# Performance work log

Hardware: AMD Instinct MI355X
Metric: run time of the kernel (lower is better)

The kernel has to match this reference:

```python
import jax, jax.numpy as jnp
from jax import lax
import numpy as np

EPS = 1e-5
N_OBS_STEPS = 2

def _layernorm(x, g, b):
    m = jnp.mean(x, -1, keepdims=True)
    v = jnp.mean((x - m) ** 2, -1, keepdims=True)
    return (x - m) * lax.rsqrt(v + EPS) * g + b

def _fps(pc, num_points):
    # pc: [B, N, 3]; iterative farthest point sampling, start at index 0
    B, N, _ = pc.shape
    dist0 = jnp.full((B, N), jnp.inf, pc.dtype)
    far0 = jnp.zeros((B,), jnp.int32)
    def step(carry, _):
        dist, far = carry
        centroid = jnp.take_along_axis(pc, far[:, None, None], axis=1)  # [B,1,3]
        d = jnp.sum((pc - centroid) ** 2, -1)                            # [B,N]
        dist = jnp.minimum(dist, d)
        nxt = jnp.argmax(dist, -1).astype(jnp.int32)
        return (dist, nxt), far
    _, idx = lax.scan(step, (dist0, far0), None, length=num_points)
    idx = idx.T  # [B, num_points]
    return jnp.take_along_axis(pc, idx[..., None], axis=1)

def setup_inputs() -> dict:
    key = jax.random.key(0)
    ks = jax.random.split(key, 16)
    B, N, S = 256, 8192, 32
    def lin(k, i, o):
        return jax.random.normal(k, (i, o), jnp.float32) / np.sqrt(i)
    inp = {
        'point_cloud': jax.random.normal(ks[0], (B, N, 3), jnp.float32),
        'joint_state': jax.random.normal(ks[1], (B, S), jnp.float32),
        'num_points': 2048,
        'w1': lin(ks[2], 3, 64),   'b1': jnp.zeros((64,)),  'g1': jnp.ones((64,)),  'be1': jnp.zeros((64,)),
        'w2': lin(ks[3], 64, 128), 'b2': jnp.zeros((128,)), 'g2': jnp.ones((128,)), 'be2': jnp.zeros((128,)),
        'w3': lin(ks[4], 128, 256),'b3': jnp.zeros((256,)), 'g3': jnp.ones((256,)), 'be3': jnp.zeros((256,)),
        'wp': lin(ks[5], 256, 64), 'bp': jnp.zeros((64,)),  'gp': jnp.ones((64,)),  'bep': jnp.zeros((64,)),
        'ws1': lin(ks[6], S, 64),  'bs1': jnp.zeros((64,)),
        'ws2': lin(ks[7], 64, 64), 'bs2': jnp.zeros((64,)),
    }
    return inp

def reference(point_cloud, joint_state, num_points,
              w1, b1, g1, be1, w2, b2, g2, be2, w3, b3, g3, be3,
              wp, bp, gp, bep, ws1, bs1, ws2, bs2):
    pc = point_cloud[..., :3]
    pc = _fps(pc, num_points)                               # [B, num_points, 3]
    # PointNet pointwise MLP: 3->64->128->256 with LN+ReLU
    h = jax.nn.relu(_layernorm(pc @ w1 + b1, g1, be1))
    h = jax.nn.relu(_layernorm(h @ w2 + b2, g2, be2))
    h = jax.nn.relu(_layernorm(h @ w3 + b3, g3, be3))
    g = jnp.max(h, axis=1)                                  # global max pool [B,256]
    global_token = _layernorm(g @ wp + bp, gp, bep)         # [B,64]
    # State MLP: S->64->64 with ReLU between
    s = jax.nn.relu(joint_state @ ws1 + bs1)
    s = s @ ws2 + bs2                                       # [B,64]
    feat = jnp.concatenate([global_token, s], axis=-1)      # [B,128]
    B = feat.shape[0] // N_OBS_STEPS
    return feat.reshape(B, -1)                              # film conditioning
```

## Files before the change

### kernel.cpp

```cpp
#include <hip/hip_runtime.h>
#include <hip/hip_bf16.h>

#define EPS 1e-5f

typedef __attribute__((ext_vector_type(8))) short short8;
typedef __attribute__((ext_vector_type(4))) float floatx4;
typedef __attribute__((ext_vector_type(2))) float f32x2;

static __device__ __forceinline__ short f2bf(float f) {
    __hip_bfloat16 h = __float2bfloat16(f);
    return *reinterpret_cast<short*>(&h);
}

__global__ __launch_bounds__(256) void prep_kernel(const float* __restrict__ w2,
                                                   const float* __restrict__ w3,
                                                   short* __restrict__ w2T,
                                                   short* __restrict__ w3T,
                                                   int* __restrict__ gmax) {
    int i = blockIdx.x * 256 + threadIdx.x;
    if (i < 8192) {
        int k = i >> 7, n = i & 127;
        w2T[n * 64 + k] = f2bf(w2[i]);
    } else if (i < 40960) {
        int j = i - 8192;
        int k = j >> 8, n = j & 255;
        w3T[n * 128 + k] = f2bf(w3[j]);
    }
    if (i < 256 * 256) gmax[i] = 0;
}

#define DPP_MAXU64(pk, CTRL, RM)                                             \
    {                                                                        \
        int lo_ = (int)(unsigned)((pk) & 0xffffffffull);                     \
        int hi_ = (int)(unsigned)((pk) >> 32);                               \
        int nlo_ = __builtin_amdgcn_update_dpp(lo_, lo_, CTRL, RM, 0xf, false); \
        int nhi_ = __builtin_amdgcn_update_dpp(hi_, hi_, CTRL, RM, 0xf, false); \
        unsigned long long o_ =                                              \
            ((unsigned long long)(unsigned)nhi_ << 32) | (unsigned)nlo_;     \
        if (o_ > (pk)) (pk) = o_;                                            \
    }

__global__ __launch_bounds__(512, 2) void fps_kernel(const float* __restrict__ pc,
                                                     float* __restrict__ sampled) {
#pragma clang fp contract(off)
    const int b = blockIdx.x;
    const int tid = threadIdx.x;
    const int wave = tid >> 6;
    const int lane = tid & 63;
    const float* __restrict__ P = pc + (size_t)b * 8192 * 3;
    float* __restrict__ outp = sampled + (size_t)b * 2048 * 3;

    __shared__ float sx[8192];
    __shared__ float sy[8192];
    __shared__ float sz[8192];
    __shared__ unsigned long long slots[2][8];

    f32x2 px2[8], py2[8], pz2[8], d2[8];
#pragma unroll
    for (int j = 0; j < 8; ++j) {
        int i0 = (2 * j) * 512 + tid;
        int i1 = (2 * j + 1) * 512 + tid;
        float x0 = P[i0 * 3 + 0], y0 = P[i0 * 3 + 1], z0 = P[i0 * 3 + 2];
        float x1 = P[i1 * 3 + 0], y1 = P[i1 * 3 + 1], z1 = P[i1 * 3 + 2];
        px2[j][0] = x0; px2[j][1] = x1;
        py2[j][0] = y0; py2[j][1] = y1;
        pz2[j][0] = z0; pz2[j][1] = z1;
        d2[j][0] = INFINITY; d2[j][1] = INFINITY;
        sx[i0] = x0; sy[i0] = y0; sz[i0] = z0;
        sx[i1] = x1; sy[i1] = y1; sz[i1] = z1;
    }
    __syncthreads();

    int far = 0;
    for (int s = 0; s < 2048; ++s) {
        const float cx = sx[far];
        const float cy = sy[far];
        const float cz = sz[far];
        if (tid == 0) {
            outp[s * 3 + 0] = cx;
            outp[s * 3 + 1] = cy;
            outp[s * 3 + 2] = cz;
        }
        if (s == 2047) break;

        const f32x2 c2x = {cx, cx}, c2y = {cy, cy}, c2z = {cz, cz};
        float bv_lo = -1.0f, bv_hi = -1.0f;
        int bj_lo = 0, bj_hi = 0;
#pragma unroll
        for (int j = 0; j < 8; ++j) {
            f32x2 dx = px2[j] - c2x;
            f32x2 dy = py2[j] - c2y;
            f32x2 dz = pz2[j] - c2z;
            f32x2 dd = (dx * dx + dy * dy) + dz * dz;
            f32x2 old = d2[j];
            f32x2 nd;
            nd[0] = fminf(old[0], dd[0]);
            nd[1] = fminf(old[1], dd[1]);
            d2[j] = nd;
            if (nd[0] > bv_lo) { bv_lo = nd[0]; bj_lo = j; }
            if (nd[1] > bv_hi) { bv_hi = nd[1]; bj_hi = j; }
        }
        float bv; int bi;
        if (bv_hi > bv_lo) { bv = bv_hi; bi = (2 * bj_hi + 1) * 512 + tid; }
        else               { bv = bv_lo; bi = (2 * bj_lo) * 512 + tid; }

        unsigned long long pk =
            ((unsigned long long)__float_as_uint(bv) << 32) | (unsigned)(8191 - bi);

        DPP_MAXU64(pk, 0x111, 0xf);
        DPP_MAXU64(pk, 0x112, 0xf);
        DPP_MAXU64(pk, 0x114, 0xf);
        DPP_MAXU64(pk, 0x118, 0xf);
        DPP_MAXU64(pk, 0x142, 0xa);
        DPP_MAXU64(pk, 0x143, 0xc);

        if (lane == 63) slots[s & 1][wave] = pk;
        __syncthreads();

        unsigned long long best = slots[s & 1][0];
#pragma unroll
        for (int k = 1; k < 8; ++k) {
            unsigned long long o = slots[s & 1][k];
            if (o > best) best = o;
        }
        far = 8191 - (int)(unsigned)(best & 0xFFFFFFFFull);
    }
}

__global__ __launch_bounds__(256) void mlp_kernel(
    const float* __restrict__ sampled,
    const float* __restrict__ w1, const float* __restrict__ b1,
    const float* __restrict__ g1, const float* __restrict__ be1,
    const short* __restrict__ w2T, const float* __restrict__ b2,
    const float* __restrict__ g2, const float* __restrict__ be2,
    const short* __restrict__ w3T, const float* __restrict__ b3,
    const float* __restrict__ g3, const float* __restrict__ be3,
    int* __restrict__ gmax) {

    const int b = blockIdx.x >> 5;
    const int chunk = blockIdx.x & 31;
    const int tid = threadIdx.x;
    const int w = tid >> 6;
    const int lane = tid & 63;
    const int quad = lane >> 4;
    const int col = lane & 15;

    __shared__ __align__(16) short X1[64 * 72];
    __shared__ __align__(16) char bufB[64 * 136 * 2];
    __shared__ float statsS[64 * 65];
    __shared__ float statsQ[64 * 65];
    __shared__ float mean_s[64];
    __shared__ float inv_s[64];

    float* Y1 = reinterpret_cast<float*>(bufB);
    short* X2 = reinterpret_cast<short*>(bufB);

    short8 b2f[2][2];
#pragma unroll
    for (int nt = 0; nt < 2; ++nt)
#pragma unroll
        for (int ks = 0; ks < 2; ++ks)
            b2f[nt][ks] = *(const short8*)&w2T[((w * 2 + nt) * 16 + col) * 64 + ks * 32 + quad * 8];
    short8 b3f[4][4];
#pragma unroll
    for (int nt = 0; nt < 4; ++nt)
#pragma unroll
        for (int ks = 0; ks < 4; ++ks)
            b3f[nt][ks] = *(const short8*)&w3T[((w * 4 + nt) * 16 + col) * 128 + ks * 32 + quad * 8];

    const int pt = tid & 63;
    const int cg = (tid >> 6) * 16;
    const float* Pp = &sampled[((size_t)b * 2048 + chunk * 64 + pt) * 3];
    const float x = Pp[0], y = Pp[1], z = Pp[2];
#pragma unroll
    for (int c = 0; c < 16; ++c) {
        int ch = cg + c;
        Y1[pt * 65 + ch] = fmaf(x, w1[ch], fmaf(y, w1[64 + ch], fmaf(z, w1[128 + ch], b1[ch])));
    }
    __syncthreads();

    if (tid < 64) {
        float s = 0.f, q = 0.f;
        for (int k = 0; k < 64; ++k) {
            float v = Y1[tid * 65 + k];
            s += v; q += v * v;
        }
        float m = s * (1.f / 64.f);
        float var = q * (1.f / 64.f) - m * m;
        mean_s[tid] = m;
        inv_s[tid] = rsqrtf(var + EPS);
    }
    __syncthreads();

#pragma unroll
    for (int c = 0; c < 16; ++c) {
        int ch = cg + c;
        float v = (Y1[pt * 65 + ch] - mean_s[pt]) * inv_s[pt] * g1[ch] + be1[ch];
        X1[pt * 72 + ch] = f2bf(fmaxf(v, 0.f));
    }
    __syncthreads();

    const floatx4 zf = {0.f, 0.f, 0.f, 0.f};
    floatx4 acc2[4][2];
#pragma unroll
    for (int mt = 0; mt < 4; ++mt) {
        acc2[mt][0] = zf; acc2[mt][1] = zf;
        short8 a[2];
#pragma unroll
        for (int ks = 0; ks < 2; ++ks)
            a[ks] = *(const short8*)&X1[(mt * 16 + col) * 72 + ks * 32 + quad * 8];
#pragma unroll
        for (int nt = 0; nt < 2; ++nt)
#pragma unroll
            for (int ks = 0; ks < 2; ++ks)
                acc2[mt][nt] = __builtin_amdgcn_mfma_f32_16x16x32_bf16(a[ks], b2f[nt][ks], acc2[mt][nt], 0, 0, 0);
    }
    int ch2[2];
    float b2v[2], g2v[2], be2v[2];
#pragma unroll
    for (int nt = 0; nt < 2; ++nt) {
        ch2[nt] = (w * 2 + nt) * 16 + col;
        b2v[nt] = b2[ch2[nt]]; g2v[nt] = g2[ch2[nt]]; be2v[nt] = be2[ch2[nt]];
    }
#pragma unroll
    for (int mt = 0; mt < 4; ++mt)
#pragma unroll
        for (int r = 0; r < 4; ++r) {
            float v0 = acc2[mt][0][r] + b2v[0];
            float v1 = acc2[mt][1][r] + b2v[1];
            acc2[mt][0][r] = v0; acc2[mt][1][r] = v1;
            int p = mt * 16 + quad * 4 + r;
            statsS[p * 65 + w * 16 + col] = v0 + v1;
            statsQ[p * 65 + w * 16 + col] = v0 * v0 + v1 * v1;
        }
    __syncthreads();
    if (tid < 64) {
        float s = 0.f, q = 0.f;
        for (int k = 0; k < 64; ++k) { s += statsS[tid * 65 + k]; q += statsQ[tid * 65 + k]; }
        float m = s * (1.f / 128.f);
        float var = q * (1.f / 128.f) - m * m;
        mean_s[tid] = m;
        inv_s[tid] = rsqrtf(var + EPS);
    }
    __syncthreads();
#pragma unroll
    for (int mt = 0; mt < 4; ++mt)
#pragma unroll
        for (int r = 0; r < 4; ++r) {
            int p = mt * 16 + quad * 4 + r;
            float m = mean_s[p], iv = inv_s[p];
#pragma unroll
            for (int nt = 0; nt < 2; ++nt) {
                float v = (acc2[mt][nt][r] - m) * iv * g2v[nt] + be2v[nt];
                X2[p * 136 + ch2[nt]] = f2bf(fmaxf(v, 0.f));
            }
        }
    __syncthreads();

    floatx4 acc3[4][4];
#pragma unroll
    for (int mt = 0; mt < 4; ++mt) {
#pragma unroll
        for (int nt = 0; nt < 4; ++nt) acc3[mt][nt] = zf;
        short8 a[4];
#pragma unroll
        for (int ks = 0; ks < 4; ++ks)
            a[ks] = *(const short8*)&X2[(mt * 16 + col) * 136 + ks * 32 + quad * 8];
#pragma unroll
        for (int nt = 0; nt < 4; ++nt)
#pragma unroll
            for (int ks = 0; ks < 4; ++ks)
                acc3[mt][nt] = __builtin_amdgcn_mfma_f32_16x16x32_bf16(a[ks], b3f[nt][ks], acc3[mt][nt], 0, 0, 0);
    }
    int ch3[4];
    float b3v[4], g3v[4], be3v[4];
#pragma unroll
    for (int nt = 0; nt < 4; ++nt) {
        ch3[nt] = (w * 4 + nt) * 16 + col;
        b3v[nt] = b3[ch3[nt]]; g3v[nt] = g3[ch3[nt]]; be3v[nt] = be3[ch3[nt]];
    }
#pragma unroll
    for (int mt = 0; mt < 4; ++mt)
#pragma unroll
        for (int r = 0; r < 4; ++r) {
            float s = 0.f, q = 0.f;
#pragma unroll
            for (int nt = 0; nt < 4; ++nt) {
                float v = acc3[mt][nt][r] + b3v[nt];
                acc3[mt][nt][r] = v;
                s += v; q += v * v;
            }
            int p = mt * 16 + quad * 4 + r;
            statsS[p * 65 + w * 16 + col] = s;
            statsQ[p * 65 + w * 16 + col] = q;
        }
    __syncthreads();
    if (tid < 64) {
        float s = 0.f, q = 0.f;
        for (int k = 0; k < 64; ++k) { s += statsS[tid * 65 + k]; q += statsQ[tid * 65 + k]; }
        float m = s * (1.f / 256.f);
        float var = q * (1.f / 256.f) - m * m;
        mean_s[tid] = m;
        inv_s[tid] = rsqrtf(var + EPS);
    }
    __syncthreads();

    float mx[4] = {0.f, 0.f, 0.f, 0.f};
#pragma unroll
    for (int mt = 0; mt < 4; ++mt)
#pragma unroll
        for (int r = 0; r < 4; ++r) {
            int p = mt * 16 + quad * 4 + r;
            float m = mean_s[p], iv = inv_s[p];
#pragma unroll
            for (int nt = 0; nt < 4; ++nt) {
                float v = (acc3[mt][nt][r] - m) * iv * g3v[nt] + be3v[nt];
                mx[nt] = fmaxf(mx[nt], fmaxf(v, 0.f));
            }
        }
#pragma unroll
    for (int nt = 0; nt < 4; ++nt) {
        float m = mx[nt];
        m = fmaxf(m, __shfl_xor(m, 16));
        m = fmaxf(m, __shfl_xor(m, 32));
        if (lane < 16)
            atomicMax(&gmax[b * 256 + ch3[nt]], __float_as_int(m));
    }
}

__global__ __launch_bounds__(64) void final_kernel(
    const float* __restrict__ g, const float* __restrict__ js,
    const float* __restrict__ wp, const float* __restrict__ bp,
    const float* __restrict__ gp, const float* __restrict__ bep,
    const float* __restrict__ ws1, const float* __restrict__ bs1,
    const float* __restrict__ ws2, const float* __restrict__ bs2,
    float* __restrict__ out) {
    const int b = blockIdx.x;
    const int c = threadIdx.x;

    const float* grow = g + b * 256;
    float acc = bp[c];
    for (int k = 0; k < 256; ++k) acc = fmaf(grow[k], wp[k * 64 + c], acc);
    float s = acc;
#pragma unroll
    for (int m = 1; m < 64; m <<= 1) s += __shfl_xor(s, m);
    float mean = s * (1.f / 64.f);
    float dc = acc - mean;
    float q = dc * dc;
#pragma unroll
    for (int m = 1; m < 64; m <<= 1) q += __shfl_xor(q, m);
    float var = q * (1.f / 64.f);
    out[b * 128 + c] = dc * rsqrtf(var + EPS) * gp[c] + bep[c];

    const float* jrow = js + b * 32;
    float h = bs1[c];
    for (int k = 0; k < 32; ++k) h = fmaf(jrow[k], ws1[k * 64 + c], h);
    h = fmaxf(h, 0.f);
    float s2 = bs2[c];
    for (int k = 0; k < 64; ++k) s2 = fmaf(__shfl(h, k), ws2[k * 64 + c], s2);
    out[b * 128 + 64 + c] = s2;
}

extern "C" void kernel_launch(void* const* d_in, const int* in_sizes, int n_in,
                              void* d_out, int out_size, void* d_ws, size_t ws_size,
                              hipStream_t stream) {
    const float* pc  = (const float*)d_in[0];
    const float* js  = (const float*)d_in[1];
    const float* w1  = (const float*)d_in[3];
    const float* b1  = (const float*)d_in[4];
    const float* g1  = (const float*)d_in[5];
    const float* be1 = (const float*)d_in[6];
    const float* w2  = (const float*)d_in[7];
    const float* b2  = (const float*)d_in[8];
    const float* g2  = (const float*)d_in[9];
    const float* be2 = (const float*)d_in[10];
    const float* w3  = (const float*)d_in[11];
    const float* b3  = (const float*)d_in[12];
    const float* g3  = (const float*)d_in[13];
    const float* be3 = (const float*)d_in[14];
    const float* wp  = (const float*)d_in[15];
    const float* bp  = (const float*)d_in[16];
    const float* gp  = (const float*)d_in[17];
    const float* bep = (const float*)d_in[18];
    const float* ws1 = (const float*)d_in[19];
    const float* bs1 = (const float*)d_in[20];
    const float* ws2 = (const float*)d_in[21];
    const float* bs2 = (const float*)d_in[22];

    char* ws = (char*)d_ws;
    float* sampled = (float*)(ws + 0);
    int*   gmax    = (int*)(ws + 6291456);
    short* w2T     = (short*)(ws + 6553600);
    short* w3T     = (short*)(ws + 6569984);

    prep_kernel<<<256, 256, 0, stream>>>(w2, w3, w2T, w3T, gmax);
    fps_kernel<<<256, 512, 0, stream>>>(pc, sampled);
    mlp_kernel<<<8192, 256, 0, stream>>>(sampled, w1, b1, g1, be1,
                                         w2T, b2, g2, be2, w3T, b3, g3, be3, gmax);
    final_kernel<<<256, 64, 0, stream>>>((const float*)gmax, js, wp, bp, gp, bep,
                                         ws1, bs1, ws2, bs2, (float*)d_out);
}
```

Measured before the change: 2.529 ms.

## Double FPS threads per batch, reduce via LDS atomicMax, buffer output in LDS

The FPS kernel now launches 1024 threads per batch instead of 512, so each thread holds 8 points instead of 16, which halves the per-step serial distance and argmax work. The cross-wave reduction changes from per-wave slots scanned by every thread to a single LDS atomicMax on a triple-buffered slot, which one thread clears two steps ahead. Sampled points are staged in LDS and written out coalesced at the end instead of one thread storing each step. The trade-offs are more waves contending at each per-step barrier, serialized atomics from 16 waves, and an extra 24KB of LDS per block.

```diff
diff --git a/kernel.cpp b/kernel.cpp
--- a/kernel.cpp
+++ b/kernel.cpp
@@ -40,12 +40,11 @@
         if (o_ > (pk)) (pk) = o_;                                            \
     }
 
-__global__ __launch_bounds__(512, 2) void fps_kernel(const float* __restrict__ pc,
-                                                     float* __restrict__ sampled) {
+__global__ __launch_bounds__(1024, 4) void fps_kernel(const float* __restrict__ pc,
+                                                      float* __restrict__ sampled) {
 #pragma clang fp contract(off)
     const int b = blockIdx.x;
     const int tid = threadIdx.x;
-    const int wave = tid >> 6;
     const int lane = tid & 63;
     const float* __restrict__ P = pc + (size_t)b * 8192 * 3;
     float* __restrict__ outp = sampled + (size_t)b * 2048 * 3;
@@ -53,13 +52,14 @@
     __shared__ float sx[8192];
     __shared__ float sy[8192];
     __shared__ float sz[8192];
-    __shared__ unsigned long long slots[2][8];
-
-    f32x2 px2[8], py2[8], pz2[8], d2[8];
-#pragma unroll
-    for (int j = 0; j < 8; ++j) {
-        int i0 = (2 * j) * 512 + tid;
-        int i1 = (2 * j + 1) * 512 + tid;
+    __shared__ float sout[2048 * 3];
+    __shared__ unsigned long long slots[3];
+
+    f32x2 px2[4], py2[4], pz2[4], d2[4];
+#pragma unroll
+    for (int j = 0; j < 4; ++j) {
+        int i0 = j * 2048 + tid;
+        int i1 = j * 2048 + 1024 + tid;
         float x0 = P[i0 * 3 + 0], y0 = P[i0 * 3 + 1], z0 = P[i0 * 3 + 2];
         float x1 = P[i1 * 3 + 0], y1 = P[i1 * 3 + 1], z1 = P[i1 * 3 + 2];
         px2[j][0] = x0; px2[j][1] = x1;
@@ -69,17 +69,19 @@
         sx[i0] = x0; sy[i0] = y0; sz[i0] = z0;
         sx[i1] = x1; sy[i1] = y1; sz[i1] = z1;
     }
+    if (tid < 3) slots[tid] = 0ull;
     __syncthreads();
 
     int far = 0;
+    int p = 0;
     for (int s = 0; s < 2048; ++s) {
         const float cx = sx[far];
         const float cy = sy[far];
         const float cz = sz[far];
         if (tid == 0) {
-            outp[s * 3 + 0] = cx;
-            outp[s * 3 + 1] = cy;
-            outp[s * 3 + 2] = cz;
+            sout[s * 3 + 0] = cx;
+            sout[s * 3 + 1] = cy;
+            sout[s * 3 + 2] = cz;
         }
         if (s == 2047) break;
 
@@ -87,7 +89,7 @@
         float bv_lo = -1.0f, bv_hi = -1.0f;
         int bj_lo = 0, bj_hi = 0;
 #pragma unroll
-        for (int j = 0; j < 8; ++j) {
+        for (int j = 0; j < 4; ++j) {
             f32x2 dx = px2[j] - c2x;
             f32x2 dy = py2[j] - c2y;
             f32x2 dz = pz2[j] - c2z;
@@ -101,8 +103,8 @@
             if (nd[1] > bv_hi) { bv_hi = nd[1]; bj_hi = j; }
         }
         float bv; int bi;
-        if (bv_hi > bv_lo) { bv = bv_hi; bi = (2 * bj_hi + 1) * 512 + tid; }
-        else               { bv = bv_lo; bi = (2 * bj_lo) * 512 + tid; }
+        if (bv_hi > bv_lo) { bv = bv_hi; bi = bj_hi * 2048 + 1024 + tid; }
+        else               { bv = bv_lo; bi = bj_lo * 2048 + tid; }
 
         unsigned long long pk =
             ((unsigned long long)__float_as_uint(bv) << 32) | (unsigned)(8191 - bi);
@@ -114,17 +116,21 @@
         DPP_MAXU64(pk, 0x142, 0xa);
         DPP_MAXU64(pk, 0x143, 0xc);
 
-        if (lane == 63) slots[s & 1][wave] = pk;
+        if (lane == 63)
+            atomicMax(&slots[p], pk);
         __syncthreads();
 
-        unsigned long long best = slots[s & 1][0];
-#pragma unroll
-        for (int k = 1; k < 8; ++k) {
-            unsigned long long o = slots[s & 1][k];
-            if (o > best) best = o;
-        }
+        unsigned long long best = slots[p];
+        if (tid == 0)
+            slots[p >= 1 ? p - 1 : 2] = 0ull;
         far = 8191 - (int)(unsigned)(best & 0xFFFFFFFFull);
-    }
+        p = (p == 2) ? 0 : p + 1;
+    }
+
+    __syncthreads();
+#pragma unroll
+    for (int i = 0; i < 6; ++i)
+        outp[i * 1024 + tid] = sout[i * 1024 + tid];
 }
 
 __global__ __launch_bounds__(256) void mlp_kernel(
@@ -394,7 +400,7 @@
     short* w3T     = (short*)(ws + 6569984);
 
     prep_kernel<<<256, 256, 0, stream>>>(w2, w3, w2T, w3T, gmax);
-    fps_kernel<<<256, 512, 0, stream>>>(pc, sampled);
+    fps_kernel<<<256, 1024, 0, stream>>>(pc, sampled);
     mlp_kernel<<<8192, 256, 0, stream>>>(sampled, w1, b1, g1, be1,
                                          w2T, b2, g2, be2, w3T, b3, g3, be3, gmax);
     final_kernel<<<256, 64, 0, stream>>>((const float*)gmax, js, wp, bp, gp, bep,
```

Measured after the change: 2.550 ms. About the same (+0.8%).
